# Kernel tuning notes

Hardware: AMD Instinct MI355X
Metric: run time of the kernel (lower is better)

The kernel has to match this reference:

```python
import jax, jax.numpy as jnp
import numpy as np

B, N, D_IMG, D_TXT, H, C = 256, 100, 1024, 768, 512, 512
NBLK = 8
EPS = 1e-5


def setup_inputs() -> dict:
    key = jax.random.key(0)
    ks = jax.random.split(key, 24)
    rn = lambda k, s, sc=0.04: jax.random.normal(k, s, jnp.float32) * sc
    return {
        "img_embedding": jax.random.normal(ks[0], (B, D_IMG), jnp.float32),
        "func_text_embedding": jax.random.normal(ks[1], (B, D_TXT), jnp.float32),
        "node_emb": jax.random.normal(ks[2], (B, N, 768), jnp.float32),
        "pos_emb": jax.random.uniform(ks[3], (B, N, 4), jnp.float32),
        # swin head
        "swinbn_g": jnp.ones((D_IMG,)), "swinbn_b": jnp.zeros((D_IMG,)),
        "swinfc_w": rn(ks[4], (H, D_IMG)), "swinfc_b": jnp.zeros((H,)),
        # text head
        "bntext_g": jnp.ones((D_TXT,)), "bntext_b": jnp.zeros((D_TXT,)),
        "fctext_w": rn(ks[5], (H, D_TXT)), "fctext_b": jnp.zeros((H,)),
        # node / bbox heads (BatchNorm1d over channel dim = max_node)
        "bngat_g": jnp.ones((N,)), "bngat_b": jnp.zeros((N,)),
        "fcgat_w": rn(ks[6], (480, 768)), "fcgat_b": jnp.zeros((480,)),
        "bnbbox_g": jnp.ones((N,)), "bnbbox_b": jnp.zeros((N,)),
        "fcbbox_w": rn(ks[7], (32, 4), 0.3), "fcbbox_b": jnp.zeros((32,)),
        # 8 stacked Rs_GCN non-local blocks (1x1 conv weights = [out,in])
        "gcn_theta_w": rn(ks[8], (NBLK, C, C)), "gcn_theta_b": jnp.zeros((NBLK, C)),
        "gcn_phi_w": rn(ks[9], (NBLK, C, C)), "gcn_phi_b": jnp.zeros((NBLK, C)),
        "gcn_g_w": rn(ks[10], (NBLK, C, C)), "gcn_g_b": jnp.zeros((NBLK, C)),
        "gcn_W_w": rn(ks[11], (NBLK, C, C)), "gcn_W_b": jnp.zeros((NBLK, C)),
        "gcn_bn_g": jnp.ones((NBLK, C)), "gcn_bn_b": jnp.zeros((NBLK, C)),
        # final classifier
        "ffbn_g": jnp.ones((3 * H,)), "ffbn_b": jnp.zeros((3 * H,)),
        "ff_w": rn(ks[12], (2, 3 * H)), "ff_b": jnp.zeros((2,)),
    }


def _bn2(x, g, b):  # BatchNorm1d on (B, C), training-mode batch stats
    m = x.mean(0)
    v = x.var(0)
    return (x - m) * jax.lax.rsqrt(v + EPS) * g + b


def _bn_ch(x, g, b):  # BatchNorm1d on (B, C, L), channel axis 1
    m = x.mean((0, 2), keepdims=True)
    v = x.var((0, 2), keepdims=True)
    return (x - m) * jax.lax.rsqrt(v + EPS) * g[None, :, None] + b[None, :, None]


def reference(img_embedding, func_text_embedding, node_emb, pos_emb,
              swinbn_g, swinbn_b, swinfc_w, swinfc_b,
              bntext_g, bntext_b, fctext_w, fctext_b,
              bngat_g, bngat_b, fcgat_w, fcgat_b,
              bnbbox_g, bnbbox_b, fcbbox_w, fcbbox_b,
              gcn_theta_w, gcn_theta_b, gcn_phi_w, gcn_phi_b,
              gcn_g_w, gcn_g_b, gcn_W_w, gcn_W_b, gcn_bn_g, gcn_bn_b,
              ffbn_g, ffbn_b, ff_w, ff_b):
    elu = jax.nn.elu
    # image branch: x = elu(swinfc(swinbn(img)))
    x = elu(_bn2(img_embedding, swinbn_g, swinbn_b) @ swinfc_w.T + swinfc_b)
    # text branch: elu(fc_text(bn_text(text)))
    ft = elu(_bn2(func_text_embedding, bntext_g, bntext_b) @ fctext_w.T + fctext_b)
    # node / bbox branches (BN over node dim, then linear over feature dim)
    h = elu(_bn_ch(node_emb, bngat_g, bngat_b) @ fcgat_w.T + fcgat_b)       # (B,N,480)
    p = elu(_bn_ch(pos_emb, bnbbox_g, bnbbox_b) @ fcbbox_w.T + fcbbox_b)    # (B,N,32)
    v = jnp.concatenate([h, p], axis=2).transpose(0, 2, 1)                  # (B,512,N)

    # 8 non-local Rs_GCN blocks
    for i in range(NBLK):
        g_v = jnp.einsum('oc,bcn->bno', gcn_g_w[i], v) + gcn_g_b[i]          # (B,N,C)
        th_v = jnp.einsum('oc,bcn->bno', gcn_theta_w[i], v) + gcn_theta_b[i]  # (B,N,C)
        ph_v = jnp.einsum('oc,bcn->bon', gcn_phi_w[i], v) + gcn_phi_b[i][:, None]  # (B,C,N)
        R = jnp.einsum('bnc,bcm->bnm', th_v, ph_v)                            # (B,N,N)
        A = jax.nn.softmax(R, axis=-1)
        y = jnp.einsum('bnm,bmc->bcn', A, g_v)                                # (B,C,N)
        Wy = jnp.einsum('oc,bcn->bon', gcn_W_w[i], y) + gcn_W_b[i][:, None]
        Wy = _bn_ch(Wy, gcn_bn_g[i], gcn_bn_b[i])
        v = Wy + v                                                            # residual

    emb = v.transpose(0, 2, 1)  # (B,N,512)
    # l2norm normalizes over dim=1 (the node dim), matching the torch code
    emb = emb / jnp.sqrt(jnp.sum(emb * emb, axis=1, keepdims=True))
    h_feature = emb.mean(axis=1)  # (B,512)

    all_feats = jnp.concatenate([x, h_feature, ft], axis=1)  # (B,1536)
    out = _bn2(all_feats, ffbn_g, ffbn_b) @ ff_w.T + ff_b    # (B,2)
    return out
```

## Files before the change

kernel.cpp:

```cpp
#include <hip/hip_runtime.h>
#include <cstddef>

#define EPS 1e-5f

constexpr int Bsz = 256;
constexpr int Nn  = 100;
constexpr int Cc  = 512;
constexpr int BN_ROWS = Bsz * Nn;

__device__ __forceinline__ void gload_lds16(const void* g, void* l) {
    __builtin_amdgcn_global_load_lds(
        (const __attribute__((address_space(1))) void*)g,
        (__attribute__((address_space(3))) void*)l, 16, 0, 0);
}

__global__ void colstats_kernel(const float* __restrict__ x, int M, int Ccols,
                                const float* __restrict__ g, const float* __restrict__ bb,
                                float* __restrict__ s, float* __restrict__ t) {
    int c = blockIdx.x;
    int r = threadIdx.x;
    float v = (r < M) ? x[(size_t)r * Ccols + c] : 0.f;
    __shared__ float ssum[256], ssq[256];
    ssum[r] = v; ssq[r] = v * v;
    __syncthreads();
    for (int off = 128; off > 0; off >>= 1) {
        if (r < off) { ssum[r] += ssum[r + off]; ssq[r] += ssq[r + off]; }
        __syncthreads();
    }
    if (r == 0) {
        float m   = ssum[0] / M;
        float var = ssq[0] / M - m * m;
        float sc  = g[c] * rsqrtf(var + EPS);
        s[c] = sc;
        t[c] = bb[c] - m * sc;
    }
}

__global__ void chstats_kernel(const float* __restrict__ x, int D,
                               const float* __restrict__ g, const float* __restrict__ bb,
                               float* __restrict__ s, float* __restrict__ t) {
    int n = blockIdx.x;
    int tid = threadIdx.x;
    int total = Bsz * D;
    float sum = 0.f, sq = 0.f;
    for (int idx = tid; idx < total; idx += blockDim.x) {
        int b = idx / D, d = idx - b * D;
        float v = x[((size_t)b * Nn + n) * D + d];
        sum += v; sq += v * v;
    }
    __shared__ float ssum[256], ssq[256];
    ssum[tid] = sum; ssq[tid] = sq;
    __syncthreads();
    for (int off = 128; off > 0; off >>= 1) {
        if (tid < off) { ssum[tid] += ssum[tid + off]; ssq[tid] += ssq[tid + off]; }
        __syncthreads();
    }
    if (tid == 0) {
        float m   = ssum[0] / total;
        float var = ssq[0] / total - m * m;
        float sc  = g[n] * rsqrtf(var + EPS);
        s[n] = sc;
        t[n] = bb[n] - m * sc;
    }
}

__global__ void chstats_part_kernel(const float* __restrict__ x, float* __restrict__ npart) {
    int n = blockIdx.x, chunk = blockIdx.y;
    int tid = threadIdx.x;
    float sum = 0.f, sq = 0.f;
    for (int i = tid; i < 3072; i += 256) {
        int rrow = i / 192;
        int q = i - rrow * 192;
        float4 f = *(const float4*)(x + ((size_t)(chunk * 16 + rrow) * Nn + n) * 768 + q * 4);
        sum += f.x + f.y + f.z + f.w;
        sq  += f.x * f.x + f.y * f.y + f.z * f.z + f.w * f.w;
    }
    __shared__ float ss[256], s2[256];
    ss[tid] = sum; s2[tid] = sq;
    __syncthreads();
    for (int off = 128; off > 0; off >>= 1) {
        if (tid < off) { ss[tid] += ss[tid + off]; s2[tid] += s2[tid + off]; }
        __syncthreads();
    }
    if (tid == 0) {
        npart[chunk * 200 + n] = ss[0];
        npart[chunk * 200 + 100 + n] = s2[0];
    }
}

__global__ void chstats_fin_kernel(const float* __restrict__ npart,
                                   const float* __restrict__ g, const float* __restrict__ bb,
                                   float* __restrict__ s, float* __restrict__ t) {
    int n = threadIdx.x;
    if (n >= 100) return;
    float sum = 0.f, sq = 0.f;
    for (int c = 0; c < 16; c++) {
        sum += npart[c * 200 + n];
        sq  += npart[c * 200 + 100 + n];
    }
    const float total = 256.f * 768.f;
    float m   = sum / total;
    float var = sq / total - m * m;
    float sc  = g[n] * rsqrtf(var + EPS);
    s[n] = sc;
    t[n] = bb[n] - m * sc;
}

__global__ void transpose_w_kernel(const float* __restrict__ w, const float* __restrict__ bias,
                                   float* __restrict__ WT, float* __restrict__ pb) {
    __shared__ float tile[32][33];
    int kb = blockIdx.x * 32, nb = blockIdx.y * 32;
    int tx = threadIdx.x & 31, ty = threadIdx.x >> 5;
#pragma unroll
    for (int i = 0; i < 4; i++) {
        int n = nb + ty + i * 8;
        tile[ty + i * 8][tx] = (n < 480) ? w[(size_t)n * 768 + kb + tx] : 0.f;
    }
    __syncthreads();
#pragma unroll
    for (int i = 0; i < 4; i++) {
        int k = kb + ty + i * 8;
        WT[(size_t)k * 512 + nb + tx] = tile[tx][ty + i * 8];
    }
    if (blockIdx.x == 0 && threadIdx.x < 32) {
        int n = nb + threadIdx.x;
        pb[n] = (n < 480) ? bias[n] : 0.f;
    }
}

template <int NORM, bool ELU, bool TB, int KS, int BYSHIFT>
__global__ __launch_bounds__(256) void gemm128_kernel(
    const float* __restrict__ A, const float* __restrict__ B0,
    const float* __restrict__ B1, int nsplit,
    const float* __restrict__ bias,
    const float* __restrict__ s, const float* __restrict__ t,
    int M, int N, int K, int lda, int ldb, int mod,
    float* __restrict__ C, int ldc, int c_off) {
    constexpr int BS = TB ? 132 : 128;
    __shared__ float As[KS * 132];
    __shared__ float Bs[KS * BS];

    int bid = blockIdx.x;
    int xcd = bid & 7;
    int l = bid >> 3;
    int by = l & ((1 << BYSHIFT) - 1);
    int bmi = l >> BYSHIFT;
    int bm_per_xcd = (int)(gridDim.x >> (3 + BYSHIFT));
    int bm = (xcd * bm_per_xcd + bmi) * 128;

    const float* B = (by < nsplit) ? B0 : B1;
    int bn = (by < nsplit ? by : by - nsplit) * 128;
    int outcol0 = c_off + by * 128;

    int tid = threadIdx.x;
    int lane = tid & 63, wave = tid >> 6;
    int tx = tid & 15, ty = tid >> 4;

    float acc[8][8] = {};

    for (int k0 = 0; k0 < K; k0 += KS) {
#pragma unroll
        for (int i = 0; i < KS / 8; i++) {
            int id = tid + i * 256;
            int row = id / (KS / 4), q = id % (KS / 4);
            int gr = bm + row;
            float4 f = *(const float4*)(A + (size_t)gr * lda + k0 + q * 4);
            if constexpr (NORM == 2) {
                int n_ = gr % mod; float sc = s[n_], sh = t[n_];
                f.x = f.x * sc + sh; f.y = f.y * sc + sh;
                f.z = f.z * sc + sh; f.w = f.w * sc + sh;
            }
            As[(q * 4 + 0) * 132 + row] = f.x;
            As[(q * 4 + 1) * 132 + row] = f.y;
            As[(q * 4 + 2) * 132 + row] = f.z;
            As[(q * 4 + 3) * 132 + row] = f.w;
        }
        if constexpr (TB) {
#pragma unroll
            for (int i = 0; i < KS / 8; i++) {
                int id = tid + i * 256;
                int row = id / (KS / 4), q = id % (KS / 4);
                int gn = bn + row;
                float4 f = make_float4(0.f, 0.f, 0.f, 0.f);
                if (gn < N) f = *(const float4*)(B + (size_t)gn * ldb + k0 + q * 4);
                Bs[(q * 4 + 0) * BS + row] = f.x;
                Bs[(q * 4 + 1) * BS + row] = f.y;
                Bs[(q * 4 + 2) * BS + row] = f.z;
                Bs[(q * 4 + 3) * BS + row] = f.w;
            }
        } else {
#pragma unroll
            for (int i = 0; i < KS / 8; i++) {
                int r = i * 8 + wave * 2 + (lane >> 5);
                gload_lds16(B + (size_t)(k0 + r) * ldb + bn + (lane & 31) * 4,
                            (char*)&Bs[r * BS]);
            }
        }
        __syncthreads();
#pragma unroll 16
        for (int kk = 0; kk < KS; kk++) {
            float4 a0 = *(const float4*)&As[kk * 132 + ty * 4];
            float4 a1 = *(const float4*)&As[kk * 132 + ty * 4 + 64];
            float4 b0 = *(const float4*)&Bs[kk * BS + tx * 4];
            float4 b1 = *(const float4*)&Bs[kk * BS + tx * 4 + 64];
            float av[8] = {a0.x, a0.y, a0.z, a0.w, a1.x, a1.y, a1.z, a1.w};
            float bv[8] = {b0.x, b0.y, b0.z, b0.w, b1.x, b1.y, b1.z, b1.w};
#pragma unroll
            for (int i = 0; i < 8; i++)
#pragma unroll
                for (int j = 0; j < 8; j++)
                    acc[i][j] = fmaf(av[i], bv[j], acc[i][j]);
        }
        __syncthreads();
    }

#pragma unroll
    for (int i = 0; i < 8; i++) {
        int r = ty * 4 + (i & 3) + ((i & 4) ? 64 : 0);
        int gr = bm + r;
        if (gr >= M) continue;
        float* crow = C + (size_t)gr * ldc + outcol0;
#pragma unroll
        for (int h = 0; h < 2; h++) {
            int cl = tx * 4 + h * 64;
            int gcol = bn + cl;
            if constexpr (TB) { if (gcol >= N) continue; }
            float4 o;
            o.x = acc[i][h * 4 + 0]; o.y = acc[i][h * 4 + 1];
            o.z = acc[i][h * 4 + 2]; o.w = acc[i][h * 4 + 3];
            if (bias) {
                o.x += bias[gcol]; o.y += bias[gcol + 1];
                o.z += bias[gcol + 2]; o.w += bias[gcol + 3];
            }
            if constexpr (ELU) {
                o.x = o.x > 0.f ? o.x : expm1f(o.x);
                o.y = o.y > 0.f ? o.y : expm1f(o.y);
                o.z = o.z > 0.f ? o.z : expm1f(o.z);
                o.w = o.w > 0.f ? o.w : expm1f(o.w);
            }
            *(float4*)(crow + cl) = o;
        }
    }
}

template <int NORM, bool ELU, bool TB>
__global__ void gemm_kernel(const float* __restrict__ A, const float* __restrict__ B,
                            const float* __restrict__ bias,
                            const float* __restrict__ s, const float* __restrict__ t,
                            int M, int N, int K, int lda, int ldb, int mod,
                            float* __restrict__ Cout, int ldc, int c_off) {
    __shared__ float As[16][65];
    __shared__ float Bs[16][65];

    int bm = blockIdx.x * 64, bn = blockIdx.y * 64;
    int tid = threadIdx.x;
    int tm = (tid >> 4) << 2;
    int tn = (tid & 15) << 2;
    float acc[4][4] = {};

    for (int k0 = 0; k0 < K; k0 += 16) {
#pragma unroll
        for (int i = 0; i < 4; i++) {
            int idx = tid + i * 256;
            {
                int rr = idx >> 4, kk = idx & 15;
                int gr = bm + rr, gk = k0 + kk;
                float av = 0.f;
                if (gr < M && gk < K) {
                    av = A[(size_t)gr * lda + gk];
                    if constexpr (NORM == 1) av = av * s[gk] + t[gk];
                    else if constexpr (NORM == 2) { int n_ = gr % mod; av = av * s[n_] + t[n_]; }
                }
                As[kk][rr] = av;
            }
            if constexpr (TB) {
                int nn = idx >> 4, kk = idx & 15;
                int gn = bn + nn, gk = k0 + kk;
                Bs[kk][nn] = (gn < N && gk < K) ? B[(size_t)gn * ldb + gk] : 0.f;
            } else {
                int kk = idx >> 6, nn = idx & 63;
                int gn = bn + nn, gk = k0 + kk;
                Bs[kk][nn] = (gn < N && gk < K) ? B[(size_t)gk * ldb + gn] : 0.f;
            }
        }
        __syncthreads();
#pragma unroll
        for (int kk = 0; kk < 16; kk++) {
            float a0[4], b0[4];
#pragma unroll
            for (int i = 0; i < 4; i++) a0[i] = As[kk][tm + i];
#pragma unroll
            for (int j = 0; j < 4; j++) b0[j] = Bs[kk][tn + j];
#pragma unroll
            for (int i = 0; i < 4; i++)
#pragma unroll
                for (int j = 0; j < 4; j++)
                    acc[i][j] = fmaf(a0[i], b0[j], acc[i][j]);
        }
        __syncthreads();
    }

#pragma unroll
    for (int i = 0; i < 4; i++) {
        int gr = bm + tm + i;
        if (gr >= M) continue;
#pragma unroll
        for (int j = 0; j < 4; j++) {
            int gn = bn + tn + j;
            if (gn >= N) continue;
            float v = acc[i][j] + (bias ? bias[gn] : 0.f);
            if constexpr (ELU) v = v > 0.f ? v : expm1f(v);
            Cout[(size_t)gr * ldc + c_off + gn] = v;
        }
    }
}

__global__ __launch_bounds__(256) void compose_kernel(
    const float* __restrict__ thw, const float* __restrict__ phw,
    const float* __restrict__ gw, const float* __restrict__ Ww,
    float* __restrict__ Mw_all, float* __restrict__ WGT_all) {
    __shared__ float As[32][33];
    __shared__ float Bs[32][68];
    int blk = blockIdx.z >> 1;
    int z = blockIdx.z & 1;
    size_t woff = (size_t)blk * Cc * Cc;
    const float* A = (z ? gw : thw) + woff;
    const float* ph = phw + woff;
    const float* W = Ww + woff;
    int bm = blockIdx.x * 32, bn = blockIdx.y * 64;
    int tid = threadIdx.x;
    int tm = (tid >> 4) * 2, tn = (tid & 15) * 4;
    float acc[2][4] = {};

    for (int k0 = 0; k0 < Cc; k0 += 32) {
#pragma unroll
        for (int i = 0; i < 4; i++) {
            int id = tid + i * 256;
            int kk = id >> 5, m = id & 31;
            As[kk][m] = A[(size_t)(k0 + kk) * Cc + bm + m];
        }
#pragma unroll
        for (int i = 0; i < 8; i++) {
            int id = tid + i * 256;
            if (z == 0) {
                int kk = id >> 6, n = id & 63;
                Bs[kk][n] = ph[(size_t)(k0 + kk) * Cc + bn + n];
            } else {
                int n = id >> 5, kk = id & 31;
                Bs[kk][n] = W[(size_t)(bn + n) * Cc + k0 + kk];
            }
        }
        __syncthreads();
#pragma unroll
        for (int kk = 0; kk < 32; kk++) {
            float a0 = As[kk][tm], a1 = As[kk][tm + 1];
            float4 b4 = *(const float4*)&Bs[kk][tn];
            acc[0][0] = fmaf(a0, b4.x, acc[0][0]);
            acc[0][1] = fmaf(a0, b4.y, acc[0][1]);
            acc[0][2] = fmaf(a0, b4.z, acc[0][2]);
            acc[0][3] = fmaf(a0, b4.w, acc[0][3]);
            acc[1][0] = fmaf(a1, b4.x, acc[1][0]);
            acc[1][1] = fmaf(a1, b4.y, acc[1][1]);
            acc[1][2] = fmaf(a1, b4.z, acc[1][2]);
            acc[1][3] = fmaf(a1, b4.w, acc[1][3]);
        }
        __syncthreads();
    }
    float* out = (z ? WGT_all : Mw_all) + woff;
    *(float4*)&out[(size_t)(bm + tm) * Cc + bn + tn] =
        make_float4(acc[0][0], acc[0][1], acc[0][2], acc[0][3]);
    *(float4*)&out[(size_t)(bm + tm + 1) * Cc + bn + tn] =
        make_float4(acc[1][0], acc[1][1], acc[1][2], acc[1][3]);
}

__global__ void qc_kernel(const float* __restrict__ phw, const float* __restrict__ thb,
                          const float* __restrict__ Ww, const float* __restrict__ gb,
                          const float* __restrict__ Wb,
                          float* __restrict__ q2a, float* __restrict__ cca) {
    int blk = blockIdx.y >> 1;
    int type = blockIdx.y & 1;
    int c = blockIdx.x;
    int l = threadIdx.x;
    float acc = 0.f;
    if (type == 0) {
        const float* phi = phw + (size_t)blk * Cc * Cc;
        const float* tb = thb + (size_t)blk * Cc;
        for (int j = l; j < Cc; j += 64) acc += phi[(size_t)j * Cc + c] * tb[j];
        for (int off = 32; off > 0; off >>= 1) acc += __shfl_xor(acc, off, 64);
        if (l == 0) q2a[blk * Cc + c] = acc;
    } else {
        const float* W = Ww + (size_t)blk * Cc * Cc;
        const float* gbb = gb + (size_t)blk * Cc;
        for (int j = l; j < Cc; j += 64) acc += W[(size_t)c * Cc + j] * gbb[j];
        for (int off = 32; off > 0; off >>= 1) acc += __shfl_xor(acc, off, 64);
        if (l == 0) cca[blk * Cc + c] = acc + Wb[(size_t)blk * Cc + c];
    }
}

__global__ void bbox_kernel(const float* __restrict__ pos, const float* __restrict__ w,
                            const float* __restrict__ bias, const float* __restrict__ s,
                            const float* __restrict__ t, float* __restrict__ V) {
    __shared__ float ws[32][4];
    int tid = threadIdx.x;
    if (tid < 128) ws[tid >> 2][tid & 3] = w[tid];
    __syncthreads();
    int r = blockIdx.x * 8 + (tid >> 5);
    int o = tid & 31;
    int n = r % Nn;
    float sc = s[n], sh = t[n];
    float p0 = pos[(size_t)r * 4 + 0] * sc + sh;
    float p1 = pos[(size_t)r * 4 + 1] * sc + sh;
    float p2 = pos[(size_t)r * 4 + 2] * sc + sh;
    float p3 = pos[(size_t)r * 4 + 3] * sc + sh;
    float acc = bias[o] + p0 * ws[o][0] + p1 * ws[o][1] + p2 * ws[o][2] + p3 * ws[o][3];
    acc = acc > 0.f ? acc : expm1f(acc);
    V[(size_t)r * Cc + 480 + o] = acc;
}

__global__ __launch_bounds__(256) void attn_fused_kernel(
    float* __restrict__ TZ, const float* __restrict__ V,
    const float* __restrict__ q2, const float* __restrict__ cc,
    float* __restrict__ part) {
    __shared__ float smem[11904];
    float* Ts = smem;
    float* Vs = smem + 1800;
    float* A_lds = smem;
    float* ct_lds = smem + 5400;
    float* Zs = smem + 5504;

    int bid = blockIdx.x;
    int xcd = bid & 7;
    int l = bid >> 3;
    int b = xcd * 32 + (l >> 1);
    int rh = l & 1;
    int row0 = b * Nn + rh * 50;
    int tid = threadIdx.x;
    int lane = tid & 63, wave = tid >> 6;
    int tx = tid & 31, ty = tid >> 5;

    {
        int r = tid >> 1, h = tid & 1;
        float cacc = 0.f;
        if (r < Nn) {
            const float4* vp = (const float4*)(V + (size_t)(b * Nn + r) * 512);
            const float4* qp = (const float4*)q2;
            for (int c4 = h; c4 < 128; c4 += 2) {
                float4 f = vp[c4], q = qp[c4];
                cacc += f.x * q.x + f.y * q.y + f.z * q.z + f.w * q.w;
            }
        }
        cacc += __shfl_xor(cacc, 1, 64);
        if (r < Nn && h == 0) ct_lds[r] = cacc;
    }

    float acc[7][4];
#pragma unroll
    for (int i = 0; i < 7; i++)
#pragma unroll
        for (int j = 0; j < 4; j++) acc[i][j] = 0.f;

    for (int kt = 0; kt < 16; kt++) {
        __syncthreads();
        for (int i = tid; i < 1200; i += 256) {
            if (i < 400) {
                int r = i >> 3, q = i & 7;
                float4 f = *(const float4*)(TZ + (size_t)(row0 + r) * 1024 + kt * 32 + q * 4);
                *(float4*)&Ts[r * 36 + q * 4] = f;
            } else {
                int ii = i - 400;
                int r = ii >> 3, q = ii & 7;
                float4 f = *(const float4*)(V + (size_t)(b * Nn + r) * 512 + kt * 32 + q * 4);
                *(float4*)&Vs[r * 36 + q * 4] = f;
            }
        }
        __syncthreads();
#pragma unroll
        for (int q = 0; q < 8; q++) {
            float4 av[7];
#pragma unroll
            for (int i = 0; i < 7; i++)
                av[i] = *(const float4*)&Ts[(ty * 7 + i) * 36 + q * 4];
            float4 bv[4];
#pragma unroll
            for (int j = 0; j < 4; j++)
                bv[j] = *(const float4*)&Vs[(tx + 32 * j) * 36 + q * 4];
#pragma unroll
            for (int kk = 0; kk < 4; kk++) {
#pragma unroll
                for (int i = 0; i < 7; i++) {
                    float a = ((const float*)&av[i])[kk];
#pragma unroll
                    for (int j = 0; j < 4; j++)
                        acc[i][j] = fmaf(a, ((const float*)&bv[j])[kk], acc[i][j]);
                }
            }
        }
    }
    __syncthreads();

    float ctv[4];
#pragma unroll
    for (int j = 0; j < 4; j++) {
        int c = tx + 32 * j;
        ctv[j] = (c < Nn) ? ct_lds[c] : 0.f;
    }
#pragma unroll
    for (int i = 0; i < 7; i++) {
        int r = ty * 7 + i;
        if (r >= 50) continue;
#pragma unroll
        for (int j = 0; j < 4; j++) {
            int c = tx + 32 * j;
            if (c < Nn) A_lds[r * 105 + c] = acc[i][j] + ctv[j];
        }
    }
    __syncthreads();
    if (tid < 50) {
        float* row = A_lds + tid * 105;
        float mx = -1e30f;
        for (int m = 0; m < Nn; m++) mx = fmaxf(mx, row[m]);
        float sm = 0.f;
        for (int m = 0; m < Nn; m++) { float e = expf(row[m] - mx); row[m] = e; sm += e; }
        float inv = 1.f / sm;
        for (int m = 0; m < Nn; m++) row[m] *= inv;
    }

    int pair = b * 2 + rh;
    for (int ch = 0; ch < 2; ch++) {
        float acc2[7][8];
#pragma unroll
        for (int i = 0; i < 7; i++)
#pragma unroll
            for (int j = 0; j < 8; j++) acc2[i][j] = 0.f;

        for (int kt = 0; kt < 4; kt++) {
            __syncthreads();
            for (int r = wave; r < 25; r += 4) {
                gload_lds16(TZ + (size_t)(b * Nn + kt * 25 + r) * 1024 + 512 + ch * 256 + lane * 4,
                            (char*)&Zs[r * 256]);
            }
            __syncthreads();
#pragma unroll 5
            for (int k2 = 0; k2 < 25; k2++) {
                int k = kt * 25 + k2;
                float av[7];
#pragma unroll
                for (int i = 0; i < 7; i++) av[i] = A_lds[(ty * 7 + i) * 105 + k];
                float zv[8];
#pragma unroll
                for (int j = 0; j < 8; j++) zv[j] = Zs[k2 * 256 + tx + 32 * j];
#pragma unroll
                for (int i = 0; i < 7; i++)
#pragma unroll
                    for (int j = 0; j < 8; j++)
                        acc2[i][j] = fmaf(av[i], zv[j], acc2[i][j]);
            }
        }

        float ccv[8];
#pragma unroll
        for (int j = 0; j < 8; j++) ccv[j] = cc[ch * 256 + tx + 32 * j];
        float psum[8], psq[8];
#pragma unroll
        for (int j = 0; j < 8; j++) { psum[j] = 0.f; psq[j] = 0.f; }
#pragma unroll
        for (int i = 0; i < 7; i++) {
            int r = ty * 7 + i;
            if (r >= 50) continue;
            float* orow = TZ + (size_t)(row0 + r) * 1024 + ch * 256;
#pragma unroll
            for (int j = 0; j < 8; j++) {
                float v = acc2[i][j] + ccv[j];
                orow[tx + 32 * j] = v;
                psum[j] += v; psq[j] += v * v;
            }
        }
        __syncthreads();
        float* sums = Zs;
#pragma unroll
        for (int j = 0; j < 8; j++) {
            int c = tx + 32 * j;
            sums[ty * 512 + c] = psum[j];
            sums[ty * 512 + 256 + c] = psq[j];
        }
        __syncthreads();
        {
            float ssv = 0.f, sqv = 0.f;
            for (int y = 0; y < 8; y++) {
                ssv += sums[y * 512 + tid];
                sqv += sums[y * 512 + 256 + tid];
            }
            part[(size_t)pair * 1024 + ch * 256 + tid] = ssv;
            part[(size_t)pair * 1024 + 512 + ch * 256 + tid] = sqv;
        }
    }
}

__global__ void wy_fin2_kernel(const float* __restrict__ part,
                               const float* __restrict__ g, const float* __restrict__ bb,
                               float* __restrict__ s, float* __restrict__ t) {
    int c = blockIdx.x;
    int l = threadIdx.x;
    float sum = 0.f, sq = 0.f;
    for (int p = l; p < 512; p += 64) {
        sum += part[(size_t)p * 1024 + c];
        sq  += part[(size_t)p * 1024 + 512 + c];
    }
    for (int off = 32; off > 0; off >>= 1) {
        sum += __shfl_xor(sum, off, 64);
        sq  += __shfl_xor(sq, off, 64);
    }
    if (l == 0) {
        float m   = sum / BN_ROWS;
        float var = sq / BN_ROWS - m * m;
        float sc  = g[c] * rsqrtf(var + EPS);
        s[c] = sc;
        t[c] = bb[c] - m * sc;
    }
}

__global__ void residual_kernel(float* __restrict__ V, const float* __restrict__ Wy, int ldw,
                                const float* __restrict__ s, const float* __restrict__ t) {
    size_t total4 = (size_t)BN_ROWS * Cc / 4;
    for (size_t i4 = (size_t)blockIdx.x * blockDim.x + threadIdx.x; i4 < total4;
         i4 += (size_t)gridDim.x * blockDim.x) {
        int row = (int)(i4 >> 7);
        int c = (int)(i4 & 127) * 4;
        float4 w = *(const float4*)(Wy + (size_t)row * ldw + c);
        float4 sv = *(const float4*)(s + c);
        float4 tv = *(const float4*)(t + c);
        float4 v = *(float4*)(V + (size_t)row * Cc + c);
        v.x += w.x * sv.x + tv.x; v.y += w.y * sv.y + tv.y;
        v.z += w.z * sv.z + tv.z; v.w += w.w * sv.w + tv.w;
        *(float4*)(V + (size_t)row * Cc + c) = v;
    }
}

__global__ void l2norm_mean_kernel(const float* __restrict__ V, float* __restrict__ ALL) {
    int b = blockIdx.x;
    int c = threadIdx.x;
    float sum = 0.f, sq = 0.f;
    const float* p = V + (size_t)b * Nn * Cc + c;
    for (int n = 0; n < Nn; n++) {
        float v = p[(size_t)n * Cc];
        sum += v; sq += v * v;
    }
    ALL[(size_t)b * 1536 + 512 + c] = sum / (Nn * sqrtf(sq));
}

__global__ void final_kernel(const float* __restrict__ ALL, const float* __restrict__ s,
                             const float* __restrict__ t, const float* __restrict__ w,
                             const float* __restrict__ bias, float* __restrict__ out) {
    int b = blockIdx.x;
    int tid = threadIdx.x;
    float p0 = 0.f, p1 = 0.f;
    for (int k = tid; k < 1536; k += 256) {
        float af = ALL[(size_t)b * 1536 + k] * s[k] + t[k];
        p0 += af * w[k];
        p1 += af * w[1536 + k];
    }
    __shared__ float s0[256], s1[256];
    s0[tid] = p0; s1[tid] = p1;
    __syncthreads();
    for (int off = 128; off > 0; off >>= 1) {
        if (tid < off) { s0[tid] += s0[tid + off]; s1[tid] += s1[tid + off]; }
        __syncthreads();
    }
    if (tid == 0) {
        out[b * 2 + 0] = s0[0] + bias[0];
        out[b * 2 + 1] = s1[0] + bias[1];
    }
}

extern "C" void kernel_launch(void* const* d_in, const int* in_sizes, int n_in,
                              void* d_out, int out_size, void* d_ws, size_t ws_size,
                              hipStream_t stream) {
    const float* img   = (const float*)d_in[0];
    const float* txt   = (const float*)d_in[1];
    const float* node  = (const float*)d_in[2];
    const float* pos   = (const float*)d_in[3];
    const float* swinbn_g = (const float*)d_in[4];
    const float* swinbn_b = (const float*)d_in[5];
    const float* swinfc_w = (const float*)d_in[6];
    const float* swinfc_b = (const float*)d_in[7];
    const float* bntext_g = (const float*)d_in[8];
    const float* bntext_b = (const float*)d_in[9];
    const float* fctext_w = (const float*)d_in[10];
    const float* fctext_b = (const float*)d_in[11];
    const float* bngat_g  = (const float*)d_in[12];
    const float* bngat_b  = (const float*)d_in[13];
    const float* fcgat_w  = (const float*)d_in[14];
    const float* fcgat_b  = (const float*)d_in[15];
    const float* bnbbox_g = (const float*)d_in[16];
    const float* bnbbox_b = (const float*)d_in[17];
    const float* fcbbox_w = (const float*)d_in[18];
    const float* fcbbox_b = (const float*)d_in[19];
    const float* gcn_theta_w = (const float*)d_in[20];
    const float* gcn_theta_b = (const float*)d_in[21];
    const float* gcn_phi_w   = (const float*)d_in[22];
    const float* gcn_phi_b   = (const float*)d_in[23];
    const float* gcn_g_w     = (const float*)d_in[24];
    const float* gcn_g_b     = (const float*)d_in[25];
    const float* gcn_W_w     = (const float*)d_in[26];
    const float* gcn_W_b     = (const float*)d_in[27];
    const float* gcn_bn_g    = (const float*)d_in[28];
    const float* gcn_bn_b    = (const float*)d_in[29];
    const float* ffbn_g = (const float*)d_in[30];
    const float* ffbn_b = (const float*)d_in[31];
    const float* ff_w   = (const float*)d_in[32];
    const float* ff_b   = (const float*)d_in[33];

    float* ws = (float*)d_ws;
    const size_t VN = (size_t)BN_ROWS * Cc;
    const size_t CC2 = (size_t)Cc * Cc;
    float* V       = ws;
    float* TZ      = V + VN;
    float* Mw_all  = TZ + VN * 2;
    float* WGT_all = Mw_all + 8 * CC2;
    float* WT      = WGT_all + 8 * CC2;
    float* ALL     = WT + 393216;
    float* part    = ALL + (size_t)Bsz * 1536;
    float* q2_all  = part + 524288;
    float* cc_all  = q2_all + 4096;
    float* st      = cc_all + 4096;
    float* s_img = st;            float* t_img = s_img + 1024;
    float* s_txt = t_img + 1024;  float* t_txt = s_txt + 768;
    float* s_nd  = t_txt + 768;   float* t_nd  = s_nd + 128;
    float* s_bb  = t_nd + 128;    float* t_bb  = s_bb + 128;
    float* s_g   = t_bb + 128;    float* t_g   = s_g + 512;
    float* s_ff  = t_g + 512;     float* t_ff  = s_ff + 1536;
    float* pb    = t_ff + 1536;

    dim3 blk(256);

    colstats_kernel<<<1024, 256, 0, stream>>>(img, 256, 1024, swinbn_g, swinbn_b, s_img, t_img);
    colstats_kernel<<<768, 256, 0, stream>>>(txt, 256, 768, bntext_g, bntext_b, s_txt, t_txt);
    chstats_part_kernel<<<dim3(100, 16, 1), 256, 0, stream>>>(node, part);
    chstats_fin_kernel<<<1, 128, 0, stream>>>(part, bngat_g, bngat_b, s_nd, t_nd);
    chstats_kernel<<<100, 256, 0, stream>>>(pos, 4, bnbbox_g, bnbbox_b, s_bb, t_bb);

    gemm_kernel<1, true, true><<<dim3(4, 8, 1), blk, 0, stream>>>(
        img, swinfc_w, swinfc_b, s_img, t_img, 256, 512, 1024, 1024, 1024, 0,
        ALL, 1536, 0);
    gemm_kernel<1, true, true><<<dim3(4, 8, 1), blk, 0, stream>>>(
        txt, fctext_w, fctext_b, s_txt, t_txt, 256, 512, 768, 768, 768, 0,
        ALL, 1536, 1024);
    transpose_w_kernel<<<dim3(24, 16, 1), blk, 0, stream>>>(fcgat_w, fcgat_b, WT, pb);
    gemm128_kernel<2, true, false, 32, 2><<<800, blk, 0, stream>>>(
        node, WT, nullptr, 4, pb, s_nd, t_nd,
        25600, 512, 768, 768, 512, 100, V, 512, 0);
    bbox_kernel<<<3200, 256, 0, stream>>>(pos, fcbbox_w, fcbbox_b, s_bb, t_bb, V);

    compose_kernel<<<dim3(16, 8, 16), blk, 0, stream>>>(
        gcn_theta_w, gcn_phi_w, gcn_g_w, gcn_W_w, Mw_all, WGT_all);
    qc_kernel<<<dim3(512, 16, 1), 64, 0, stream>>>(
        gcn_phi_w, gcn_theta_b, gcn_W_w, gcn_g_b, gcn_W_b, q2_all, cc_all);

    for (int i = 0; i < 8; i++) {
        gemm128_kernel<0, false, false, 32, 3><<<1600, blk, 0, stream>>>(
            V, Mw_all + (size_t)i * CC2, WGT_all + (size_t)i * CC2, 4,
            nullptr, nullptr, nullptr,
            25600, 1024, 512, 512, 512, 0, TZ, 1024, 0);

        attn_fused_kernel<<<512, blk, 0, stream>>>(
            TZ, V, q2_all + (size_t)i * Cc, cc_all + (size_t)i * Cc, part);

        wy_fin2_kernel<<<512, 64, 0, stream>>>(part, gcn_bn_g + (size_t)i * Cc,
                                               gcn_bn_b + (size_t)i * Cc, s_g, t_g);
        residual_kernel<<<2048, 256, 0, stream>>>(V, TZ, 1024, s_g, t_g);
    }

    l2norm_mean_kernel<<<256, 512, 0, stream>>>(V, ALL);
    colstats_kernel<<<1536, 256, 0, stream>>>(ALL, 256, 1536, ffbn_g, ffbn_b, s_ff, t_ff);
    final_kernel<<<256, 256, 0, stream>>>(ALL, s_ff, t_ff, ff_w, ff_b, (float*)d_out);
}
```

Measured before the change: 4.678 ms.

## Use 128x256 GEMM tile for per-block projections and fuse final residual into l2norm

```diff
diff --git a/kernel.cpp b/kernel.cpp
--- a/kernel.cpp
+++ b/kernel.cpp
@@ -159,6 +159,14 @@
     float acc[8][8] = {};
 
     for (int k0 = 0; k0 < K; k0 += KS) {
+        if constexpr (!TB) {
+#pragma unroll
+            for (int i = 0; i < KS / 8; i++) {
+                int r = i * 8 + wave * 2 + (lane >> 5);
+                gload_lds16(B + (size_t)(k0 + r) * ldb + bn + (lane & 31) * 4,
+                            (char*)&Bs[r * BS]);
+            }
+        }
 #pragma unroll
         for (int i = 0; i < KS / 8; i++) {
             int id = tid + i * 256;
@@ -188,13 +196,6 @@
                 Bs[(q * 4 + 2) * BS + row] = f.z;
                 Bs[(q * 4 + 3) * BS + row] = f.w;
             }
-        } else {
-#pragma unroll
-            for (int i = 0; i < KS / 8; i++) {
-                int r = i * 8 + wave * 2 + (lane >> 5);
-                gload_lds16(B + (size_t)(k0 + r) * ldb + bn + (lane & 31) * 4,
-                            (char*)&Bs[r * BS]);
-            }
         }
         __syncthreads();
 #pragma unroll 16
@@ -239,6 +240,86 @@
                 o.w = o.w > 0.f ? o.w : expm1f(o.w);
             }
             *(float4*)(crow + cl) = o;
+        }
+    }
+}
+
+template <int KS>
+__global__ __launch_bounds__(256) void gemm256_kernel(
+    const float* __restrict__ A, const float* __restrict__ B0,
+    const float* __restrict__ B1, int nsplit,
+    int M, int K, int lda, int ldb,
+    float* __restrict__ C, int ldc) {
+    __shared__ float As[KS * 132];
+    __shared__ float Bs[KS * 260];
+
+    int bid = blockIdx.x;
+    int xcd = bid & 7;
+    int l = bid >> 3;
+    int by = l & 3;
+    int bmi = l >> 2;
+    int bm_per_xcd = (int)(gridDim.x >> 5);
+    int bm = (xcd * bm_per_xcd + bmi) * 128;
+
+    const float* B = (by < nsplit) ? B0 : B1;
+    int bn = (by < nsplit ? by : by - nsplit) * 256;
+    int outcol0 = by * 256;
+
+    int tid = threadIdx.x;
+    int lane = tid & 63, wave = tid >> 6;
+    int tx = tid & 15, ty = tid >> 4;
+
+    float acc[8][16] = {};
+
+    for (int k0 = 0; k0 < K; k0 += KS) {
+#pragma unroll
+        for (int i = 0; i < KS / 4; i++) {
+            int r = i * 4 + wave;
+            gload_lds16(B + (size_t)(k0 + r) * ldb + bn + lane * 4,
+                        (char*)&Bs[r * 260]);
+        }
+#pragma unroll
+        for (int i = 0; i < KS / 8; i++) {
+            int id = tid + i * 256;
+            int row = id / (KS / 4), q = id % (KS / 4);
+            float4 f = *(const float4*)(A + (size_t)(bm + row) * lda + k0 + q * 4);
+            As[(q * 4 + 0) * 132 + row] = f.x;
+            As[(q * 4 + 1) * 132 + row] = f.y;
+            As[(q * 4 + 2) * 132 + row] = f.z;
+            As[(q * 4 + 3) * 132 + row] = f.w;
+        }
+        __syncthreads();
+#pragma unroll 4
+        for (int kk = 0; kk < KS; kk++) {
+            float4 a0 = *(const float4*)&As[kk * 132 + ty * 4];
+            float4 a1 = *(const float4*)&As[kk * 132 + ty * 4 + 64];
+            float4 b0 = *(const float4*)&Bs[kk * 260 + tx * 4];
+            float4 b1 = *(const float4*)&Bs[kk * 260 + tx * 4 + 64];
+            float4 b2 = *(const float4*)&Bs[kk * 260 + tx * 4 + 128];
+            float4 b3 = *(const float4*)&Bs[kk * 260 + tx * 4 + 192];
+            float av[8] = {a0.x, a0.y, a0.z, a0.w, a1.x, a1.y, a1.z, a1.w};
+            float bv[16] = {b0.x, b0.y, b0.z, b0.w, b1.x, b1.y, b1.z, b1.w,
+                            b2.x, b2.y, b2.z, b2.w, b3.x, b3.y, b3.z, b3.w};
+#pragma unroll
+            for (int i = 0; i < 8; i++)
+#pragma unroll
+                for (int j = 0; j < 16; j++)
+                    acc[i][j] = fmaf(av[i], bv[j], acc[i][j]);
+        }
+        __syncthreads();
+    }
+
+#pragma unroll
+    for (int i = 0; i < 8; i++) {
+        int r = ty * 4 + (i & 3) + ((i & 4) ? 64 : 0);
+        int gr = bm + r;
+        float* crow = C + (size_t)gr * ldc + outcol0;
+#pragma unroll
+        for (int h = 0; h < 4; h++) {
+            float4 o;
+            o.x = acc[i][h * 4 + 0]; o.y = acc[i][h * 4 + 1];
+            o.z = acc[i][h * 4 + 2]; o.w = acc[i][h * 4 + 3];
+            *(float4*)(crow + tx * 4 + h * 64) = o;
         }
     }
 }
@@ -636,13 +717,17 @@
     }
 }
 
-__global__ void l2norm_mean_kernel(const float* __restrict__ V, float* __restrict__ ALL) {
+__global__ void l2norm_mean_kernel(const float* __restrict__ V, const float* __restrict__ TZwy,
+                                   const float* __restrict__ s, const float* __restrict__ t,
+                                   float* __restrict__ ALL) {
     int b = blockIdx.x;
     int c = threadIdx.x;
+    float sc = s[c], sh = t[c];
     float sum = 0.f, sq = 0.f;
     const float* p = V + (size_t)b * Nn * Cc + c;
+    const float* w = TZwy + (size_t)b * Nn * 1024 + c;
     for (int n = 0; n < Nn; n++) {
-        float v = p[(size_t)n * Cc];
+        float v = p[(size_t)n * Cc] + w[(size_t)n * 1024] * sc + sh;
         sum += v; sq += v * v;
     }
     ALL[(size_t)b * 1536 + 512 + c] = sum / (Nn * sqrtf(sq));
@@ -715,7 +800,7 @@
     const size_t CC2 = (size_t)Cc * Cc;
     float* V       = ws;
     float* TZ      = V + VN;
-    float* Mw_all  = TZ + VN * 2;
+    float* Mw_all  = TZ + 2 * VN;
     float* WGT_all = Mw_all + 8 * CC2;
     float* WT      = WGT_all + 8 * CC2;
     float* ALL     = WT + 393216;
@@ -757,20 +842,21 @@
         gcn_phi_w, gcn_theta_b, gcn_W_w, gcn_g_b, gcn_W_b, q2_all, cc_all);
 
     for (int i = 0; i < 8; i++) {
-        gemm128_kernel<0, false, false, 32, 3><<<1600, blk, 0, stream>>>(
-            V, Mw_all + (size_t)i * CC2, WGT_all + (size_t)i * CC2, 4,
-            nullptr, nullptr, nullptr,
-            25600, 1024, 512, 512, 512, 0, TZ, 1024, 0);
+        gemm256_kernel<32><<<800, blk, 0, stream>>>(
+            V, Mw_all + (size_t)i * CC2, WGT_all + (size_t)i * CC2, 2,
+            25600, 512, 512, 512, TZ, 1024);
 
         attn_fused_kernel<<<512, blk, 0, stream>>>(
             TZ, V, q2_all + (size_t)i * Cc, cc_all + (size_t)i * Cc, part);
 
         wy_fin2_kernel<<<512, 64, 0, stream>>>(part, gcn_bn_g + (size_t)i * Cc,
                                                gcn_bn_b + (size_t)i * Cc, s_g, t_g);
-        residual_kernel<<<2048, 256, 0, stream>>>(V, TZ, 1024, s_g, t_g);
-    }
-
-    l2norm_mean_kernel<<<256, 512, 0, stream>>>(V, ALL);
+
+        if (i < 7)
+            residual_kernel<<<4096, 256, 0, stream>>>(V, TZ, 1024, s_g, t_g);
+    }
+
+    l2norm_mean_kernel<<<256, 512, 0, stream>>>(V, TZ, s_g, t_g, ALL);
     colstats_kernel<<<1536, 256, 0, stream>>>(ALL, 256, 1536, ffbn_g, ffbn_b, s_ff, t_ff);
     final_kernel<<<256, 256, 0, stream>>>(ALL, s_ff, t_ff, ff_w, ff_b, (float*)d_out);
 }
```

Measured after the change: 4.900 ms. 1.05x slower.
